# Optimization experiments

Measured on AMD Instinct MI355X. Metric: run time of the kernel, lower is better.

## Reference

```python
import jax, jax.numpy as jnp
import numpy as np

B = 65536
N_BRANCH = 54


def setup_inputs() -> dict:
    key = jax.random.key(0)
    ks = jax.random.split(key, 16)

    def xavier(k, shape):
        fan_in, fan_out = shape[-2], shape[-1]
        limit = float(np.sqrt(6.0 / (fan_in + fan_out)))
        return jax.random.uniform(k, shape, jnp.float32, -limit, limit)

    inp = {
        "x": jax.random.normal(ks[0], (B, 58), jnp.float32),
        "C_w1": xavier(ks[1], (4, 128)),   "C_b1": jnp.zeros((128,), jnp.float32),
        "C_w2": xavier(ks[2], (128, 3)),   "C_b2": jnp.zeros((3,), jnp.float32),
        "N_w1": xavier(ks[3], (54, 128)),  "N_b1": jnp.zeros((128,), jnp.float32),
        "N_w2": xavier(ks[4], (128, 54)),  "N_b2": jnp.zeros((54,), jnp.float32),
        "F_w1": xavier(ks[5], (57, 128)),  "F_b1": jnp.zeros((128,), jnp.float32),
        "F_w2": xavier(ks[6], (128, 57)),  "F_b2": jnp.zeros((57,), jnp.float32),
        "O_w1": xavier(ks[7], (N_BRANCH, 57, 128)), "O_b1": jnp.zeros((N_BRANCH, 128), jnp.float32),
        "O_w2": xavier(ks[8], (N_BRANCH, 128, 3)),  "O_b2": jnp.zeros((N_BRANCH, 3), jnp.float32),
    }
    return inp


def _mlp(x, w1, b1, w2, b2):
    return jax.nn.relu(x @ w1 + b1) @ w2 + b2


def reference(x, C_w1, C_b1, C_w2, C_b2, N_w1, N_b1, N_w2, N_b2,
              F_w1, F_b1, F_w2, F_b2, O_w1, O_b1, O_w2, O_b2):
    c_in, n_in = x[:, :4], x[:, 4:]              # [B,4], [B,54]
    c = _mlp(c_in, C_w1, C_b1, C_w2, C_b2)        # [B,3]
    n = _mlp(n_in, N_w1, N_b1, N_w2, N_b2)        # [B,54]
    f = jnp.concatenate([c, n], axis=1)           # [B,57]
    f = _mlp(f, F_w1, F_b1, F_w2, F_b2)           # [B,57]
    # All 54 O-net branches as one batched GEMM.
    h = jax.nn.relu(jnp.einsum("bc,ncd->nbd", f, O_w1) + O_b1[:, None, :])  # [54,B,128]
    logits = jnp.einsum("nbd,nde->nbe", h, O_w2) + O_b2[:, None, :]          # [54,B,3]
    probs = jax.nn.softmax(logits, axis=-1)       # softmax over the 3 classes per branch
    out = jnp.transpose(probs, (1, 0, 2)).reshape(x.shape[0], N_BRANCH * 3)  # [B,162]
    return out
```

## Files before the change

kernel.cpp:

```cpp
#include <hip/hip_runtime.h>
#include <hip/hip_bf16.h>
#include <stdint.h>

typedef __bf16 bf16;
typedef bf16 bf16x8 __attribute__((ext_vector_type(8)));
typedef float f32x4 __attribute__((ext_vector_type(4)));

#define MFMA(a, b, c) __builtin_amdgcn_mfma_f32_16x16x32_bf16((a), (b), (c), 0, 0, 0)

__device__ __forceinline__ int mk(int k) {
  return 32*(k>>5) + 16*((k>>2)&1) + 4*((k>>3)&3) + (k&3);
}


__global__ __launch_bounds__(256) void prep_kernel(
    const float* __restrict__ Cw1, const float* __restrict__ Cb1,
    const float* __restrict__ Cw2, const float* __restrict__ Cb2,
    const float* __restrict__ Nw1, const float* __restrict__ Nb1,
    const float* __restrict__ Nw2, const float* __restrict__ Nb2,
    const float* __restrict__ Fw1, const float* __restrict__ Fb1,
    const float* __restrict__ Fw2, const float* __restrict__ Fb2,
    const float* __restrict__ Ow1, const float* __restrict__ Ob1,
    const float* __restrict__ Ow2,
    bf16* __restrict__ O1T, bf16* __restrict__ O2T,
    bf16* __restrict__ blobG, float* __restrict__ bias64,
    float* __restrict__ Fb2pad)
{
  int gid = blockIdx.x * 256 + threadIdx.x;
  if (gid < 442368) {
    int m  = gid & 127;
    int k  = (gid >> 7) & 63;
    int br = gid >> 13;
    int c  = ((m >> 5) << 5) | (((m >> 2) & 3) << 3) | (((m >> 4) & 1) << 2) | (m & 3);
    float v = 0.f;
    if (k < 57)       v = Ow1[(br * 57 + k) * 128 + c];
    else if (k == 57) v = Ob1[br * 128 + c];
    O1T[(br * 128 + m) * 64 + k] = (bf16)v;
    return;
  }
  gid -= 442368;
  if (gid < 20736) {
    int br  = gid / 384;
    int rem = gid - br * 384;
    int e   = rem >> 7;
    int cc  = rem & 127;
    O2T[gid] = (bf16)Ow2[(br * 128 + cc) * 3 + e];
    return;
  }
  gid -= 20736;
  if (gid < 71680) {
    int idx = gid;
    float w = 0.f;
    bool lo = false;
    if (idx < 16384) {
      lo = idx >= 8192; int l = idx & 8191;
      int j = l >> 6, cp = l & 63;
      int k = (((cp >> 3) ^ (j & 7)) << 3) | (cp & 7);
      if (k < 54) w = Nw1[k * 128 + j];
      else if (k == 54) w = Nb1[j];
    } else if (idx < 20480) {
      int l = idx - 16384;
      int j = l >> 5, cp = l & 31;
      int kl = (((cp >> 3) ^ (j & 3)) << 3) | (cp & 7);
      int s = 32 + kl;
      if (s == 54) w = Cb1[j];
      else if (s >= 56 && s <= 59) w = Cw1[(s - 56) * 128 + j];
    } else if (idx < 36864) {
      int l = idx - 20480; lo = l >= 8192; l &= 8191;
      int o = l >> 7, cp = l & 127;
      int k = (((cp >> 3) ^ (o & 7)) << 3) | (cp & 7);
      int p = mk(k);
      if (o < 54) w = Nw2[p * 54 + o];
    } else if (idx < 38912) {
      int l = idx - 36864;
      int o = l >> 7, cp = l & 127;
      int k = (((cp >> 3) ^ (o & 7)) << 3) | (cp & 7);
      int p = mk(k);
      if (o >= 6 && o <= 8) w = Cw2[p * 3 + (o - 6)];
    } else if (idx < 55296) {
      int l = idx - 38912; lo = l >= 8192; l &= 8191;
      int j = l >> 6, cp = l & 63;
      int k = (((cp >> 3) ^ (j & 7)) << 3) | (cp & 7);
      int p = mk(k);
      if (p < 54) w = Fw1[(3 + p) * 128 + j];
      else if (p < 57) w = Fw1[(p - 54) * 128 + j];
      else if (p == 57) w = Fb1[j];
    } else {
      int l = idx - 55296; lo = l >= 8192; l &= 8191;
      int o = l >> 7, cp = l & 127;
      int k = (((cp >> 3) ^ (o & 7)) << 3) | (cp & 7);
      int p = mk(k);
      if (o < 57) w = Fw2[p * 57 + o];
    }
    bf16 h = (bf16)w;
    blobG[gid] = lo ? (bf16)(w - (float)h) : h;
    return;
  }
  gid -= 71680;
  if (gid < 64) {
    float v = 0.f;
    if (gid < 54) v = Nb2[gid];
    else if (gid < 57) v = Cb2[gid - 54];
    else if (gid == 57) v = 1.0f;
    bias64[gid] = v;
    return;
  }
  gid -= 64;
  if (gid < 64) { Fb2pad[gid] = (gid < 57) ? Fb2[gid] : 0.f; return; }
}

__global__ __launch_bounds__(512)
void mlp_kernel(
    const float* __restrict__ x, const bf16* __restrict__ blobG,
    const float* __restrict__ bias64, const float* __restrict__ Fb2pad,
    bf16* __restrict__ fbf)
{
  __shared__ bf16 blob[71680];
  const int tid = threadIdx.x;
  {
    const uint4* src = (const uint4*)blobG;
    uint4* dst = (uint4*)blob;
    for (int t = tid; t < 8960; t += 512) dst[t] = src[t];
  }
  __syncthreads();

  const int wave = tid >> 6;
  const int lane = tid & 63;
  const int lr = lane & 15;
  const int g = lane >> 4;
  const f32x4 zero4 = {0.f, 0.f, 0.f, 0.f};

  auto frag = [&](int base, int stride, int row_, int chunk, int mask) -> bf16x8 {
    int c = chunk ^ (row_ & mask);
    return *(const bf16x8*)(blob + base + row_ * stride + c * 8);
  };

#pragma unroll 1
  for (int it = 0; it < 2; ++it) {
    const int row = blockIdx.x * 256 + (it * 8 + wave) * 16 + lr;
    const float* xr = x + (size_t)row * 58;

    bf16x8 bxh[2], bxl[2];
#pragma unroll
    for (int ks = 0; ks < 2; ++ks) {
#pragma unroll
      for (int u = 0; u < 8; ++u) {
        int s = ks * 32 + g * 8 + u;
        float v;
        if (s < 54) v = xr[4 + s];
        else if (s == 54) v = 1.0f;
        else if (s >= 56 && s <= 59) v = xr[s - 56];
        else v = 0.0f;
        bf16 h = (bf16)v;
        bxh[ks][u] = h;
        bxl[ks][u] = (bf16)(v - (float)h);
      }
    }

    f32x4 acc2[4];
#pragma unroll
    for (int mt = 0; mt < 4; ++mt)
      acc2[mt] = *(const f32x4*)(bias64 + mt * 16 + 4 * g);
#pragma unroll 1
    for (int ks = 0; ks < 4; ++ks) {
      f32x4 aN[2], aC[2];
#pragma unroll
      for (int h = 0; h < 2; ++h) {
        const int mt = 2 * ks + h;
        f32x4 a = zero4;
#pragma unroll
        for (int k2 = 0; k2 < 2; ++k2) {
          bf16x8 aH = frag(0,    64, mt * 16 + lr, k2 * 4 + g, 7);
          bf16x8 aL = frag(8192, 64, mt * 16 + lr, k2 * 4 + g, 7);
          a = MFMA(aH, bxh[k2], a);
          a = MFMA(aH, bxl[k2], a);
          a = MFMA(aL, bxh[k2], a);
        }
        aN[h] = a;
        bf16x8 c8 = frag(16384, 32, mt * 16 + lr, g, 3);
        f32x4 c = MFMA(c8, bxh[1], zero4);
        c = MFMA(c8, bxl[1], c);
        aC[h] = c;
      }
      bf16x8 nh, nl, ch, cl;
#pragma unroll
      for (int u = 0; u < 8; ++u) {
        float vN = fmaxf(aN[u >> 2][u & 3], 0.f);
        bf16 hN = (bf16)vN;
        nh[u] = hN;
        nl[u] = (bf16)(vN - (float)hN);
        float vC = fmaxf(aC[u >> 2][u & 3], 0.f);
        bf16 hC = (bf16)vC;
        ch[u] = hC;
        cl[u] = (bf16)(vC - (float)hC);
      }
#pragma unroll
      for (int mt = 0; mt < 4; ++mt) {
        bf16x8 aH = frag(20480, 128, mt * 16 + lr, ks * 4 + g, 7);
        bf16x8 aL = frag(28672, 128, mt * 16 + lr, ks * 4 + g, 7);
        acc2[mt] = MFMA(aH, nh, acc2[mt]);
        acc2[mt] = MFMA(aH, nl, acc2[mt]);
        acc2[mt] = MFMA(aL, nh, acc2[mt]);
      }
      bf16x8 aCc = frag(36864, 128, lr, ks * 4 + g, 7);
      acc2[3] = MFMA(aCc, ch, acc2[3]);
      acc2[3] = MFMA(aCc, cl, acc2[3]);
    }

    bf16x8 b2fh[2], b2fl[2];
#pragma unroll
    for (int s = 0; s < 2; ++s) {
#pragma unroll
      for (int u = 0; u < 8; ++u) {
        float v = acc2[2 * s + (u >> 2)][u & 3];
        bf16 h = (bf16)v;
        b2fh[s][u] = h;
        b2fl[s][u] = (bf16)(v - (float)h);
      }
    }

    f32x4 accO[4];
#pragma unroll
    for (int mt = 0; mt < 4; ++mt)
      accO[mt] = *(const f32x4*)(Fb2pad + mt * 16 + 4 * g);
#pragma unroll 1
    for (int ks = 0; ks < 4; ++ks) {
      f32x4 aF[2];
#pragma unroll
      for (int h = 0; h < 2; ++h) {
        const int mt = 2 * ks + h;
        f32x4 a = zero4;
#pragma unroll
        for (int k2 = 0; k2 < 2; ++k2) {
          bf16x8 aH = frag(38912, 64, mt * 16 + lr, k2 * 4 + g, 7);
          bf16x8 aL = frag(47104, 64, mt * 16 + lr, k2 * 4 + g, 7);
          a = MFMA(aH, b2fh[k2], a);
          a = MFMA(aH, b2fl[k2], a);
          a = MFMA(aL, b2fh[k2], a);
        }
        aF[h] = a;
      }
      bf16x8 bh, bl;
#pragma unroll
      for (int u = 0; u < 8; ++u) {
        float v = fmaxf(aF[u >> 2][u & 3], 0.f);
        bf16 h = (bf16)v;
        bh[u] = h;
        bl[u] = (bf16)(v - (float)h);
      }
#pragma unroll
      for (int mt = 0; mt < 4; ++mt) {
        bf16x8 aH = frag(55296, 128, mt * 16 + lr, ks * 4 + g, 7);
        bf16x8 aL = frag(63488, 128, mt * 16 + lr, ks * 4 + g, 7);
        accO[mt] = MFMA(aH, bh, accO[mt]);
        accO[mt] = MFMA(aH, bl, accO[mt]);
        accO[mt] = MFMA(aL, bh, accO[mt]);
      }
    }
    if (g == 2) accO[3][1] = 1.0f;

#pragma unroll
    for (int mt = 0; mt < 4; ++mt) {
      uint32_t w0 = (uint32_t)__builtin_bit_cast(uint16_t, (bf16)accO[mt][0]) |
                    ((uint32_t)__builtin_bit_cast(uint16_t, (bf16)accO[mt][1]) << 16);
      uint32_t w1 = (uint32_t)__builtin_bit_cast(uint16_t, (bf16)accO[mt][2]) |
                    ((uint32_t)__builtin_bit_cast(uint16_t, (bf16)accO[mt][3]) << 16);
      *(uint2*)(fbf + (size_t)row * 64 + mt * 16 + 4 * g) = make_uint2(w0, w1);
    }
  }
}

template<bool USE_TMP>
__global__ __launch_bounds__(64, 3) void heads_kernel(
    const bf16* __restrict__ fbf, const bf16* __restrict__ O1T,
    const bf16* __restrict__ O2T, const float* __restrict__ Ob2,
    float* __restrict__ tmp, float* __restrict__ out)
{
  const int bid = blockIdx.x;
  const int br = bid % 54;
  const int chunk = bid / 54;
  const int lane = threadIdx.x;
  const int lr = lane & 15;
  const int g = lane >> 4;
  const f32x4 zero4 = {0.f, 0.f, 0.f, 0.f};

  const bf16* a1p = O1T + br * 8192 + lr * 64 + g * 8;
  bf16x8 a1[8][2];
#pragma unroll
  for (int mt = 0; mt < 8; ++mt)
#pragma unroll
    for (int ks = 0; ks < 2; ++ks)
      a1[mt][ks] = *(const bf16x8*)(a1p + mt * 1024 + ks * 32);

  const int e_clamp = (lr < 2) ? lr : 2;
  const bf16* w2p = O2T + br * 384 + e_clamp * 128 + g * 8;
  bf16x8 w2[4];
#pragma unroll
  for (int s2 = 0; s2 < 4; ++s2) w2[s2] = *(const bf16x8*)(w2p + s2 * 32);

  const float b0 = Ob2[br * 3 + 0], b1 = Ob2[br * 3 + 1], b2s = Ob2[br * 3 + 2];
  const float LOG2E = 1.4426950408889634f;

  const bf16* fp0 = fbf + ((size_t)(chunk * 1024 + lr)) * 64 + g * 8;
  bf16x8 fb0 = *(const bf16x8*)(fp0);
  bf16x8 fb1 = *(const bf16x8*)(fp0 + 32);

#pragma unroll 1
  for (int it = 0; it < 64; ++it) {
    const int nit = (it + 1) & 63;
    const bf16* np = fbf + ((size_t)(chunk * 1024 + nit * 16 + lr)) * 64 + g * 8;
    bf16x8 nf0 = *(const bf16x8*)(np);
    bf16x8 nf1 = *(const bf16x8*)(np + 32);

    f32x4 l2 = zero4;
#pragma unroll
    for (int s2 = 0; s2 < 4; ++s2) {
      f32x4 aA = MFMA(a1[2 * s2][0], fb0, zero4);
      f32x4 aB = MFMA(a1[2 * s2 + 1][0], fb0, zero4);
      aA = MFMA(a1[2 * s2][1], fb1, aA);
      aB = MFMA(a1[2 * s2 + 1][1], fb1, aB);
      bf16x8 b2;
#pragma unroll
      for (int t = 0; t < 4; ++t) {
        b2[t]     = (bf16)fmaxf(aA[t], 0.f);
        b2[4 + t] = (bf16)fmaxf(aB[t], 0.f);
      }
      l2 = MFMA(w2[s2], b2, l2);
    }

    const int row = chunk * 1024 + it * 16 + lr;
    float l0 = l2[0] + b0;
    float l1 = l2[1] + b1;
    float lv = l2[2] + b2s;
    float m = fmaxf(fmaxf(l0, l1), lv);
    float p0 = exp2f((l0 - m) * LOG2E);
    float p1 = exp2f((l1 - m) * LOG2E);
    float p2 = exp2f((lv - m) * LOG2E);
    float rs = __builtin_amdgcn_rcpf(p0 + p1 + p2);
    if (g == 0) {
      if (USE_TMP) {
        float* tp = tmp + ((size_t)br * 65536 + row) * 3;
        tp[0] = p0 * rs; tp[1] = p1 * rs; tp[2] = p2 * rs;
      } else {
        float* op = out + (size_t)row * 162 + br * 3;
        op[0] = p0 * rs; op[1] = p1 * rs; op[2] = p2 * rs;
      }
    }
    fb0 = nf0; fb1 = nf1;
  }
}

__global__ __launch_bounds__(256) void transpose_kernel(
    const float* __restrict__ tmp, float* __restrict__ out)
{
  __shared__ float sh[64 * 163];
  const int tid = threadIdx.x;
  const int rowbase = blockIdx.x * 64;
  for (int t = tid; t < 10368; t += 256) {
    int p = t / 192;
    int q = t - p * 192;
    int r = q / 3;
    int e = q - r * 3;
    sh[r * 163 + p * 3 + e] = tmp[((size_t)p * 65536 + rowbase + r) * 3 + e];
  }
  __syncthreads();
  for (int t = tid; t < 10368; t += 256) {
    int r = t / 162;
    int c = t - r * 162;
    out[(size_t)(rowbase + r) * 162 + c] = sh[r * 163 + c];
  }
}

extern "C" void kernel_launch(void* const* d_in, const int* in_sizes, int n_in,
                              void* d_out, int out_size, void* d_ws, size_t ws_size,
                              hipStream_t stream)
{
  (void)in_sizes; (void)n_in; (void)out_size;
  const float* x   = (const float*)d_in[0];
  const float* Cw1 = (const float*)d_in[1];
  const float* Cb1 = (const float*)d_in[2];
  const float* Cw2 = (const float*)d_in[3];
  const float* Cb2 = (const float*)d_in[4];
  const float* Nw1 = (const float*)d_in[5];
  const float* Nb1 = (const float*)d_in[6];
  const float* Nw2 = (const float*)d_in[7];
  const float* Nb2 = (const float*)d_in[8];
  const float* Fw1 = (const float*)d_in[9];
  const float* Fb1 = (const float*)d_in[10];
  const float* Fw2 = (const float*)d_in[11];
  const float* Fb2 = (const float*)d_in[12];
  const float* Ow1 = (const float*)d_in[13];
  const float* Ob1 = (const float*)d_in[14];
  const float* Ow2 = (const float*)d_in[15];
  const float* Ob2 = (const float*)d_in[16];

  char* ws = (char*)d_ws;
  bf16*  fbf    = (bf16*)(ws + 0);
  bf16*  O1T    = (bf16*)(ws + 8388608);
  bf16*  O2T    = (bf16*)(ws + 9273344);
  bf16*  blobG  = (bf16*)(ws + 9314816);
  float* bias64 = (float*)(ws + 9458176);
  float* Fb2pad = (float*)(ws + 9458432);
  float* tmp    = (float*)(ws + 9458688);
  const size_t need = 9458688ull + 42467328ull;
  const bool useTmp = ws_size >= need;

  prep_kernel<<<2090, 256, 0, stream>>>(Cw1, Cb1, Cw2, Cb2, Nw1, Nb1, Nw2, Nb2,
                                        Fw1, Fb1, Fw2, Fb2, Ow1, Ob1, Ow2,
                                        O1T, O2T, blobG, bias64, Fb2pad);
  mlp_kernel<<<256, 512, 0, stream>>>(x, blobG, bias64, Fb2pad, fbf);
  if (useTmp) {
    heads_kernel<true><<<3456, 64, 0, stream>>>(fbf, O1T, O2T, Ob2, tmp, (float*)d_out);
    transpose_kernel<<<1024, 256, 0, stream>>>(tmp, (float*)d_out);
  } else {
    heads_kernel<false><<<3456, 64, 0, stream>>>(fbf, O1T, O2T, Ob2, tmp, (float*)d_out);
  }
}
```

Before: 241.2 us.

## Split x conversion into prep, double grid sizes, fold log2e into head weights

```diff
diff --git a/kernel.cpp b/kernel.cpp
--- a/kernel.cpp
+++ b/kernel.cpp
@@ -5,8 +5,15 @@
 typedef __bf16 bf16;
 typedef bf16 bf16x8 __attribute__((ext_vector_type(8)));
 typedef float f32x4 __attribute__((ext_vector_type(4)));
+typedef uint32_t u32x4 __attribute__((ext_vector_type(4)));
 
 #define MFMA(a, b, c) __builtin_amdgcn_mfma_f32_16x16x32_bf16((a), (b), (c), 0, 0, 0)
+
+__device__ __forceinline__ uint32_t cvt_pk_bf16(float lo, float hi) {
+  uint32_t r;
+  asm("v_cvt_pk_bf16_f32 %0, %1, %2" : "=v"(r) : "v"(lo), "v"(hi));
+  return r;
+}
 
 __device__ __forceinline__ int mk(int k) {
   return 32*(k>>5) + 16*((k>>2)&1) + 4*((k>>3)&3) + (k&3);
@@ -14,6 +21,7 @@
 
 
 __global__ __launch_bounds__(256) void prep_kernel(
+    const float* __restrict__ x,
     const float* __restrict__ Cw1, const float* __restrict__ Cb1,
     const float* __restrict__ Cw2, const float* __restrict__ Cb2,
     const float* __restrict__ Nw1, const float* __restrict__ Nb1,
@@ -24,8 +32,9 @@
     const float* __restrict__ Ow2,
     bf16* __restrict__ O1T, bf16* __restrict__ O2T,
     bf16* __restrict__ blobG, float* __restrict__ bias64,
-    float* __restrict__ Fb2pad)
+    float* __restrict__ Fb2pad, bf16* __restrict__ xhi, bf16* __restrict__ xlo)
 {
+  const float LOG2E = 1.4426950408889634f;
   int gid = blockIdx.x * 256 + threadIdx.x;
   if (gid < 442368) {
     int m  = gid & 127;
@@ -44,7 +53,7 @@
     int rem = gid - br * 384;
     int e   = rem >> 7;
     int cc  = rem & 127;
-    O2T[gid] = (bf16)Ow2[(br * 128 + cc) * 3 + e];
+    O2T[gid] = (bf16)(Ow2[(br * 128 + cc) * 3 + e] * LOG2E);
     return;
   }
   gid -= 20736;
@@ -107,11 +116,33 @@
   }
   gid -= 64;
   if (gid < 64) { Fb2pad[gid] = (gid < 57) ? Fb2[gid] : 0.f; return; }
+  gid -= 64;
+  if (gid < 524288) {
+    int row = gid >> 3;
+    int s0 = (gid & 7) * 8;
+    const float* xr = x + (size_t)row * 58;
+    bf16x8 h8, l8;
+#pragma unroll
+    for (int u = 0; u < 8; ++u) {
+      int s = s0 + u;
+      float v;
+      if (s < 54) v = xr[4 + s];
+      else if (s == 54) v = 1.0f;
+      else if (s >= 56 && s <= 59) v = xr[s - 56];
+      else v = 0.0f;
+      bf16 h = (bf16)v;
+      h8[u] = h;
+      l8[u] = (bf16)(v - (float)h);
+    }
+    *(bf16x8*)(xhi + (size_t)row * 64 + s0) = h8;
+    *(bf16x8*)(xlo + (size_t)row * 64 + s0) = l8;
+  }
 }
 
 __global__ __launch_bounds__(512)
 void mlp_kernel(
-    const float* __restrict__ x, const bf16* __restrict__ blobG,
+    const bf16* __restrict__ xhi, const bf16* __restrict__ xlo,
+    const bf16* __restrict__ blobG,
     const float* __restrict__ bias64, const float* __restrict__ Fb2pad,
     bf16* __restrict__ fbf)
 {
@@ -135,147 +166,131 @@
     return *(const bf16x8*)(blob + base + row_ * stride + c * 8);
   };
 
+  const int row = blockIdx.x * 128 + wave * 16 + lr;
+
+  bf16x8 bxh[2], bxl[2];
+  bxh[0] = *(const bf16x8*)(xhi + (size_t)row * 64 + g * 8);
+  bxh[1] = *(const bf16x8*)(xhi + (size_t)row * 64 + 32 + g * 8);
+  bxl[0] = *(const bf16x8*)(xlo + (size_t)row * 64 + g * 8);
+  bxl[1] = *(const bf16x8*)(xlo + (size_t)row * 64 + 32 + g * 8);
+
+  f32x4 acc2[4];
+#pragma unroll
+  for (int mt = 0; mt < 4; ++mt)
+    acc2[mt] = *(const f32x4*)(bias64 + mt * 16 + 4 * g);
 #pragma unroll 1
-  for (int it = 0; it < 2; ++it) {
-    const int row = blockIdx.x * 256 + (it * 8 + wave) * 16 + lr;
-    const float* xr = x + (size_t)row * 58;
-
-    bf16x8 bxh[2], bxl[2];
-#pragma unroll
-    for (int ks = 0; ks < 2; ++ks) {
-#pragma unroll
-      for (int u = 0; u < 8; ++u) {
-        int s = ks * 32 + g * 8 + u;
-        float v;
-        if (s < 54) v = xr[4 + s];
-        else if (s == 54) v = 1.0f;
-        else if (s >= 56 && s <= 59) v = xr[s - 56];
-        else v = 0.0f;
-        bf16 h = (bf16)v;
-        bxh[ks][u] = h;
-        bxl[ks][u] = (bf16)(v - (float)h);
+  for (int ks = 0; ks < 4; ++ks) {
+    f32x4 aN[2], aC[2];
+#pragma unroll
+    for (int h = 0; h < 2; ++h) {
+      const int mt = 2 * ks + h;
+      f32x4 a = zero4;
+#pragma unroll
+      for (int k2 = 0; k2 < 2; ++k2) {
+        bf16x8 aH = frag(0,    64, mt * 16 + lr, k2 * 4 + g, 7);
+        bf16x8 aL = frag(8192, 64, mt * 16 + lr, k2 * 4 + g, 7);
+        a = MFMA(aH, bxh[k2], a);
+        a = MFMA(aH, bxl[k2], a);
+        a = MFMA(aL, bxh[k2], a);
       }
-    }
-
-    f32x4 acc2[4];
-#pragma unroll
-    for (int mt = 0; mt < 4; ++mt)
-      acc2[mt] = *(const f32x4*)(bias64 + mt * 16 + 4 * g);
+      aN[h] = a;
+      bf16x8 c8 = frag(16384, 32, mt * 16 + lr, g, 3);
+      f32x4 c = MFMA(c8, bxh[1], zero4);
+      c = MFMA(c8, bxl[1], c);
+      aC[h] = c;
+    }
+    bf16x8 nh, nl, ch, cl;
+#pragma unroll
+    for (int u = 0; u < 8; ++u) {
+      float vN = fmaxf(aN[u >> 2][u & 3], 0.f);
+      bf16 hN = (bf16)vN;
+      nh[u] = hN;
+      nl[u] = (bf16)(vN - (float)hN);
+      float vC = fmaxf(aC[u >> 2][u & 3], 0.f);
+      bf16 hC = (bf16)vC;
+      ch[u] = hC;
+      cl[u] = (bf16)(vC - (float)hC);
+    }
+#pragma unroll
+    for (int mt = 0; mt < 4; ++mt) {
+      bf16x8 aH = frag(20480, 128, mt * 16 + lr, ks * 4 + g, 7);
+      bf16x8 aL = frag(28672, 128, mt * 16 + lr, ks * 4 + g, 7);
+      acc2[mt] = MFMA(aH, nh, acc2[mt]);
+      acc2[mt] = MFMA(aH, nl, acc2[mt]);
+      acc2[mt] = MFMA(aL, nh, acc2[mt]);
+    }
+    bf16x8 aCc = frag(36864, 128, lr, ks * 4 + g, 7);
+    acc2[3] = MFMA(aCc, ch, acc2[3]);
+    acc2[3] = MFMA(aCc, cl, acc2[3]);
+  }
+
+  bf16x8 b2fh[2], b2fl[2];
+#pragma unroll
+  for (int s = 0; s < 2; ++s) {
+#pragma unroll
+    for (int u = 0; u < 8; ++u) {
+      float v = acc2[2 * s + (u >> 2)][u & 3];
+      bf16 h = (bf16)v;
+      b2fh[s][u] = h;
+      b2fl[s][u] = (bf16)(v - (float)h);
+    }
+  }
+
+  f32x4 accO[4];
+#pragma unroll
+  for (int mt = 0; mt < 4; ++mt)
+    accO[mt] = *(const f32x4*)(Fb2pad + mt * 16 + 4 * g);
 #pragma unroll 1
-    for (int ks = 0; ks < 4; ++ks) {
-      f32x4 aN[2], aC[2];
-#pragma unroll
-      for (int h = 0; h < 2; ++h) {
-        const int mt = 2 * ks + h;
-        f32x4 a = zero4;
-#pragma unroll
-        for (int k2 = 0; k2 < 2; ++k2) {
-          bf16x8 aH = frag(0,    64, mt * 16 + lr, k2 * 4 + g, 7);
-          bf16x8 aL = frag(8192, 64, mt * 16 + lr, k2 * 4 + g, 7);
-          a = MFMA(aH, bxh[k2], a);
-          a = MFMA(aH, bxl[k2], a);
-          a = MFMA(aL, bxh[k2], a);
-        }
-        aN[h] = a;
-        bf16x8 c8 = frag(16384, 32, mt * 16 + lr, g, 3);
-        f32x4 c = MFMA(c8, bxh[1], zero4);
-        c = MFMA(c8, bxl[1], c);
-        aC[h] = c;
+  for (int ks = 0; ks < 4; ++ks) {
+    f32x4 aF[2];
+#pragma unroll
+    for (int h = 0; h < 2; ++h) {
+      const int mt = 2 * ks + h;
+      f32x4 a = zero4;
+#pragma unroll
+      for (int k2 = 0; k2 < 2; ++k2) {
+        bf16x8 aH = frag(38912, 64, mt * 16 + lr, k2 * 4 + g, 7);
+        bf16x8 aL = frag(47104, 64, mt * 16 + lr, k2 * 4 + g, 7);
+        a = MFMA(aH, b2fh[k2], a);
+        a = MFMA(aH, b2fl[k2], a);
+        a = MFMA(aL, b2fh[k2], a);
       }
-      bf16x8 nh, nl, ch, cl;
-#pragma unroll
-      for (int u = 0; u < 8; ++u) {
-        float vN = fmaxf(aN[u >> 2][u & 3], 0.f);
-        bf16 hN = (bf16)vN;
-        nh[u] = hN;
-        nl[u] = (bf16)(vN - (float)hN);
-        float vC = fmaxf(aC[u >> 2][u & 3], 0.f);
-        bf16 hC = (bf16)vC;
-        ch[u] = hC;
-        cl[u] = (bf16)(vC - (float)hC);
-      }
-#pragma unroll
-      for (int mt = 0; mt < 4; ++mt) {
-        bf16x8 aH = frag(20480, 128, mt * 16 + lr, ks * 4 + g, 7);
-        bf16x8 aL = frag(28672, 128, mt * 16 + lr, ks * 4 + g, 7);
-        acc2[mt] = MFMA(aH, nh, acc2[mt]);
-        acc2[mt] = MFMA(aH, nl, acc2[mt]);
-        acc2[mt] = MFMA(aL, nh, acc2[mt]);
-      }
-      bf16x8 aCc = frag(36864, 128, lr, ks * 4 + g, 7);
-      acc2[3] = MFMA(aCc, ch, acc2[3]);
-      acc2[3] = MFMA(aCc, cl, acc2[3]);
-    }
-
-    bf16x8 b2fh[2], b2fl[2];
-#pragma unroll
-    for (int s = 0; s < 2; ++s) {
-#pragma unroll
-      for (int u = 0; u < 8; ++u) {
-        float v = acc2[2 * s + (u >> 2)][u & 3];
-        bf16 h = (bf16)v;
-        b2fh[s][u] = h;
-        b2fl[s][u] = (bf16)(v - (float)h);
-      }
-    }
-
-    f32x4 accO[4];
-#pragma unroll
-    for (int mt = 0; mt < 4; ++mt)
-      accO[mt] = *(const f32x4*)(Fb2pad + mt * 16 + 4 * g);
-#pragma unroll 1
-    for (int ks = 0; ks < 4; ++ks) {
-      f32x4 aF[2];
-#pragma unroll
-      for (int h = 0; h < 2; ++h) {
-        const int mt = 2 * ks + h;
-        f32x4 a = zero4;
-#pragma unroll
-        for (int k2 = 0; k2 < 2; ++k2) {
-          bf16x8 aH = frag(38912, 64, mt * 16 + lr, k2 * 4 + g, 7);
-          bf16x8 aL = frag(47104, 64, mt * 16 + lr, k2 * 4 + g, 7);
-          a = MFMA(aH, b2fh[k2], a);
-          a = MFMA(aH, b2fl[k2], a);
-          a = MFMA(aL, b2fh[k2], a);
-        }
-        aF[h] = a;
-      }
-      bf16x8 bh, bl;
-#pragma unroll
-      for (int u = 0; u < 8; ++u) {
-        float v = fmaxf(aF[u >> 2][u & 3], 0.f);
-        bf16 h = (bf16)v;
-        bh[u] = h;
-        bl[u] = (bf16)(v - (float)h);
-      }
-#pragma unroll
-      for (int mt = 0; mt < 4; ++mt) {
-        bf16x8 aH = frag(55296, 128, mt * 16 + lr, ks * 4 + g, 7);
-        bf16x8 aL = frag(63488, 128, mt * 16 + lr, ks * 4 + g, 7);
-        accO[mt] = MFMA(aH, bh, accO[mt]);
-        accO[mt] = MFMA(aH, bl, accO[mt]);
-        accO[mt] = MFMA(aL, bh, accO[mt]);
-      }
-    }
-    if (g == 2) accO[3][1] = 1.0f;
-
+      aF[h] = a;
+    }
+    bf16x8 bh, bl;
+#pragma unroll
+    for (int u = 0; u < 8; ++u) {
+      float v = fmaxf(aF[u >> 2][u & 3], 0.f);
+      bf16 h = (bf16)v;
+      bh[u] = h;
+      bl[u] = (bf16)(v - (float)h);
+    }
 #pragma unroll
     for (int mt = 0; mt < 4; ++mt) {
-      uint32_t w0 = (uint32_t)__builtin_bit_cast(uint16_t, (bf16)accO[mt][0]) |
-                    ((uint32_t)__builtin_bit_cast(uint16_t, (bf16)accO[mt][1]) << 16);
-      uint32_t w1 = (uint32_t)__builtin_bit_cast(uint16_t, (bf16)accO[mt][2]) |
-                    ((uint32_t)__builtin_bit_cast(uint16_t, (bf16)accO[mt][3]) << 16);
-      *(uint2*)(fbf + (size_t)row * 64 + mt * 16 + 4 * g) = make_uint2(w0, w1);
-    }
+      bf16x8 aH = frag(55296, 128, mt * 16 + lr, ks * 4 + g, 7);
+      bf16x8 aL = frag(63488, 128, mt * 16 + lr, ks * 4 + g, 7);
+      accO[mt] = MFMA(aH, bh, accO[mt]);
+      accO[mt] = MFMA(aH, bl, accO[mt]);
+      accO[mt] = MFMA(aL, bh, accO[mt]);
+    }
+  }
+  if (g == 2) accO[3][1] = 1.0f;
+
+#pragma unroll
+  for (int mt = 0; mt < 4; ++mt) {
+    uint32_t w0 = cvt_pk_bf16(accO[mt][0], accO[mt][1]);
+    uint32_t w1 = cvt_pk_bf16(accO[mt][2], accO[mt][3]);
+    *(uint2*)(fbf + (size_t)row * 64 + mt * 16 + 4 * g) = make_uint2(w0, w1);
   }
 }
 
 template<bool USE_TMP>
-__global__ __launch_bounds__(64, 3) void heads_kernel(
+__global__ __launch_bounds__(64, 8) void heads_kernel(
     const bf16* __restrict__ fbf, const bf16* __restrict__ O1T,
     const bf16* __restrict__ O2T, const float* __restrict__ Ob2,
     float* __restrict__ tmp, float* __restrict__ out)
 {
+  __shared__ bf16 w2s[384];
   const int bid = blockIdx.x;
   const int br = bid % 54;
   const int chunk = bid / 54;
@@ -284,6 +299,8 @@
   const int g = lane >> 4;
   const f32x4 zero4 = {0.f, 0.f, 0.f, 0.f};
 
+  if (lane < 48) ((uint4*)w2s)[lane] = ((const uint4*)(O2T + br * 384))[lane];
+
   const bf16* a1p = O1T + br * 8192 + lr * 64 + g * 8;
   bf16x8 a1[8][2];
 #pragma unroll
@@ -292,25 +309,25 @@
     for (int ks = 0; ks < 2; ++ks)
       a1[mt][ks] = *(const bf16x8*)(a1p + mt * 1024 + ks * 32);
 
+  const float LOG2E = 1.4426950408889634f;
+  const float b0 = Ob2[br * 3 + 0] * LOG2E;
+  const float b1 = Ob2[br * 3 + 1] * LOG2E;
+  const float b2s = Ob2[br * 3 + 2] * LOG2E;
+
+  __syncthreads();
   const int e_clamp = (lr < 2) ? lr : 2;
-  const bf16* w2p = O2T + br * 384 + e_clamp * 128 + g * 8;
-  bf16x8 w2[4];
-#pragma unroll
-  for (int s2 = 0; s2 < 4; ++s2) w2[s2] = *(const bf16x8*)(w2p + s2 * 32);
-
-  const float b0 = Ob2[br * 3 + 0], b1 = Ob2[br * 3 + 1], b2s = Ob2[br * 3 + 2];
-  const float LOG2E = 1.4426950408889634f;
-
-  const bf16* fp0 = fbf + ((size_t)(chunk * 1024 + lr)) * 64 + g * 8;
-  bf16x8 fb0 = *(const bf16x8*)(fp0);
-  bf16x8 fb1 = *(const bf16x8*)(fp0 + 32);
+  const bf16* w2b = w2s + e_clamp * 128 + g * 8;
+
+  const int row0 = chunk * 512 + lr;
+  const bf16* fp = fbf + (size_t)row0 * 64 + g * 8;
+  float* tp = tmp + ((size_t)br * 65536 + row0) * 3;
+  float* op = out + (size_t)row0 * 162 + br * 3;
 
 #pragma unroll 1
-  for (int it = 0; it < 64; ++it) {
-    const int nit = (it + 1) & 63;
-    const bf16* np = fbf + ((size_t)(chunk * 1024 + nit * 16 + lr)) * 64 + g * 8;
-    bf16x8 nf0 = *(const bf16x8*)(np);
-    bf16x8 nf1 = *(const bf16x8*)(np + 32);
+  for (int it = 0; it < 32; ++it) {
+    bf16x8 fb0 = *(const bf16x8*)(fp);
+    bf16x8 fb1 = *(const bf16x8*)(fp + 32);
+    fp += 1024;
 
     f32x4 l2 = zero4;
 #pragma unroll
@@ -319,34 +336,31 @@
       f32x4 aB = MFMA(a1[2 * s2 + 1][0], fb0, zero4);
       aA = MFMA(a1[2 * s2][1], fb1, aA);
       aB = MFMA(a1[2 * s2 + 1][1], fb1, aB);
-      bf16x8 b2;
-#pragma unroll
-      for (int t = 0; t < 4; ++t) {
-        b2[t]     = (bf16)fmaxf(aA[t], 0.f);
-        b2[4 + t] = (bf16)fmaxf(aB[t], 0.f);
-      }
-      l2 = MFMA(w2[s2], b2, l2);
-    }
-
-    const int row = chunk * 1024 + it * 16 + lr;
+      u32x4 bw;
+      bw[0] = cvt_pk_bf16(fmaxf(aA[0], 0.f), fmaxf(aA[1], 0.f));
+      bw[1] = cvt_pk_bf16(fmaxf(aA[2], 0.f), fmaxf(aA[3], 0.f));
+      bw[2] = cvt_pk_bf16(fmaxf(aB[0], 0.f), fmaxf(aB[1], 0.f));
+      bw[3] = cvt_pk_bf16(fmaxf(aB[2], 0.f), fmaxf(aB[3], 0.f));
+      bf16x8 w2v = *(const bf16x8*)(w2b + s2 * 32);
+      l2 = MFMA(w2v, __builtin_bit_cast(bf16x8, bw), l2);
+    }
+
     float l0 = l2[0] + b0;
     float l1 = l2[1] + b1;
     float lv = l2[2] + b2s;
     float m = fmaxf(fmaxf(l0, l1), lv);
-    float p0 = exp2f((l0 - m) * LOG2E);
-    float p1 = exp2f((l1 - m) * LOG2E);
-    float p2 = exp2f((lv - m) * LOG2E);
+    float p0 = __builtin_amdgcn_exp2f(l0 - m);
+    float p1 = __builtin_amdgcn_exp2f(l1 - m);
+    float p2 = __builtin_amdgcn_exp2f(lv - m);
     float rs = __builtin_amdgcn_rcpf(p0 + p1 + p2);
     if (g == 0) {
       if (USE_TMP) {
-        float* tp = tmp + ((size_t)br * 65536 + row) * 3;
         tp[0] = p0 * rs; tp[1] = p1 * rs; tp[2] = p2 * rs;
       } else {
-        float* op = out + (size_t)row * 162 + br * 3;
         op[0] = p0 * rs; op[1] = p1 * rs; op[2] = p2 * rs;
       }
     }
-    fb0 = nf0; fb1 = nf1;
+    if (USE_TMP) tp += 48; else op += 16 * 162;
   }
 }
 
@@ -401,18 +415,20 @@
   bf16*  blobG  = (bf16*)(ws + 9314816);
   float* bias64 = (float*)(ws + 9458176);
   float* Fb2pad = (float*)(ws + 9458432);
-  float* tmp    = (float*)(ws + 9458688);
-  const size_t need = 9458688ull + 42467328ull;
+  bf16*  xhi    = (bf16*)(ws + 9458688);
+  bf16*  xlo    = (bf16*)(ws + 17847296);
+  float* tmp    = (float*)(ws + 26235904);
+  const size_t need = 26235904ull + 42467328ull;
   const bool useTmp = ws_size >= need;
 
-  prep_kernel<<<2090, 256, 0, stream>>>(Cw1, Cb1, Cw2, Cb2, Nw1, Nb1, Nw2, Nb2,
+  prep_kernel<<<4138, 256, 0, stream>>>(x, Cw1, Cb1, Cw2, Cb2, Nw1, Nb1, Nw2, Nb2,
                                         Fw1, Fb1, Fw2, Fb2, Ow1, Ob1, Ow2,
-                                        O1T, O2T, blobG, bias64, Fb2pad);
-  mlp_kernel<<<256, 512, 0, stream>>>(x, blobG, bias64, Fb2pad, fbf);
+                                        O1T, O2T, blobG, bias64, Fb2pad, xhi, xlo);
+  mlp_kernel<<<512, 512, 0, stream>>>(xhi, xlo, blobG, bias64, Fb2pad, fbf);
   if (useTmp) {
-    heads_kernel<true><<<3456, 64, 0, stream>>>(fbf, O1T, O2T, Ob2, tmp, (float*)d_out);
+    heads_kernel<true><<<6912, 64, 0, stream>>>(fbf, O1T, O2T, Ob2, tmp, (float*)d_out);
     transpose_kernel<<<1024, 256, 0, stream>>>(tmp, (float*)d_out);
   } else {
-    heads_kernel<false><<<3456, 64, 0, stream>>>(fbf, O1T, O2T, Ob2, tmp, (float*)d_out);
-  }
-}
+    heads_kernel<false><<<6912, 64, 0, stream>>>(fbf, O1T, O2T, Ob2, tmp, (float*)d_out);
+  }
+}
```

Result: slower. 429.4 us (+78.0%).
